# Performance work log

Hardware: AMD Instinct MI355X
Metric: run time of the kernel (lower is better)

## Reference

```python
import jax, jax.numpy as jnp
import numpy as np

# Screen config (matches init_kwargs)
W, H, TL = 1920, 1080, 16
NBW = -(-W // TL)          # 120
NBH = -(-H // TL)          # 68
NB = NBW * NBH             # 8160 tiles
N = 500_000                # number of points
K = 5                      # max tiles per axis a point can overlap (radius < 24, TL=16)
RADIUS_MAX = 24.0


def setup_inputs() -> dict:
    key = jax.random.key(0)
    k1, k2, k3 = jax.random.split(key, 3)
    pos2d = jax.random.uniform(k1, (N, 2), dtype=jnp.float32) * jnp.array([W, H], dtype=jnp.float32)
    radius = jax.random.uniform(k2, (N,), dtype=jnp.float32) * (RADIUS_MAX - 1.0) + 1.0
    depth = jax.random.normal(k3, (N,), dtype=jnp.float32)
    return {"pos2d": pos2d, "radius": radius, "depth": depth}


def reference(pos2d, radius, depth):
    # Tile bounds per point (identical clamping semantics to the torch module).
    xmin = jnp.clip(jnp.floor_divide(pos2d[:, 0] - radius, TL), 0, NBW).astype(jnp.int32)
    ymin = jnp.clip(jnp.floor_divide(pos2d[:, 1] - radius, TL), 0, NBH).astype(jnp.int32)
    xmax = jnp.clip(jnp.floor_divide(pos2d[:, 0] + radius, TL) + 1, 0, NBW).astype(jnp.int32)
    ymax = jnp.clip(jnp.floor_divide(pos2d[:, 1] + radius, TL) + 1, 0, NBH).astype(jnp.int32)

    # Enumerate a fixed KxK candidate tile window per point, mask out-of-range tiles.
    dxy = jnp.arange(K, dtype=jnp.int32)
    xi = xmin[:, None] + dxy            # [N, K]
    yi = ymin[:, None] + dxy            # [N, K]
    vx = xi < xmax[:, None]
    vy = yi < ymax[:, None]
    valid = (vx[:, :, None] & vy[:, None, :]).reshape(-1)              # [E]
    tid = (xi[:, :, None] * NBH + yi[:, None, :]).reshape(-1)          # [E] flat tile id (x-major, as in module)
    tid = jnp.where(valid, tid, NB).astype(jnp.int32)                  # sentinel NB -> sorts to end
    pid = jnp.broadcast_to(jnp.arange(N, dtype=jnp.int32)[:, None, None], (N, K, K)).reshape(-1)
    d_entry = jnp.broadcast_to(depth[:, None, None], (N, K, K)).reshape(-1)

    # Counting-sort equivalent: per-tile histogram + exclusive cumsum offsets.
    counts = jax.ops.segment_sum(valid.astype(jnp.int32), tid, num_segments=NB + 1)[:NB]
    tile_count = jnp.concatenate([jnp.zeros((1,), jnp.int32), jnp.cumsum(counts)[:-1].astype(jnp.int32)])

    # Sort pairs by (tile id, depth descending) -> contiguous per-tile, depth-sorted index lists.
    order = jnp.lexsort((-d_entry, tid))
    tid_s = tid[order]
    pid_s = pid[order]
    live = tid_s < NB
    tile_indices = jnp.where(live, pid_s, -1)                          # padded with -1 at the tail
    sorted_depth = jnp.where(live, depth[pid_s], 0.0)                  # depths in per-tile sorted order
    return tile_count, tile_indices, sorted_depth
```

## Files before the change

### kernel.cpp

```cpp
#include <hip/hip_runtime.h>
#include <stdint.h>
#include <math.h>

typedef unsigned int u32;
typedef unsigned long long u64;

#define NBW 120
#define NBH 68
#define NTILES (NBW * NBH)
#define NPTS 500000
#define EE 12500000
#define SORT_CAP 2048
#define NBKT 1024
#define HB 256
#define HT 512
#define DX 121
#define DY 69
#define DCELLS 8352
#define PCW 4080
#define DSLICE (HB * DCELLS)
#define PCSLICE (HB * PCW)

__device__ __forceinline__ int clampi(int v, int lo, int hi) {
    return v < lo ? lo : (v > hi ? hi : v);
}

__device__ __forceinline__ void tile_window(float x, float y, float r,
                                            int& x0, int& x1, int& y0, int& y1) {
    x0 = clampi((int)floorf((x - r) * 0.0625f), 0, NBW);
    x1 = clampi((int)floorf((x + r) * 0.0625f) + 1, 0, NBW);
    y0 = clampi((int)floorf((y - r) * 0.0625f), 0, NBH);
    y1 = clampi((int)floorf((y + r) * 0.0625f) + 1, 0, NBH);
}

__device__ __forceinline__ u32 depth_key(float d) {
    u32 fu = __float_as_uint(d);
    u32 asc = (fu & 0x80000000u) ? ~fu : (fu | 0x80000000u);
    return ~asc;
}
__device__ __forceinline__ float depth_unkey(u32 dk) {
    u32 asc = ~dk;
    u32 fu = (asc & 0x80000000u) ? (asc & 0x7FFFFFFFu) : ~asc;
    return __uint_as_float(fu);
}

__device__ __forceinline__ int tile_of_block(int b) {
    return (b & 7) * (NTILES / 8) + (b >> 3);
}

__device__ __forceinline__ u32 bucket_of(u32 dk, const u32* __restrict__ Ts) {
    u32 k = dk >> 24;
    u32 t0 = Ts[k], t1 = Ts[k + 1];
    u32 b = t0 + (((t1 - t0) * ((dk >> 8) & 0xFFFFu)) >> 16);
    return b >= NBKT ? (NBKT - 1) : b;
}

__device__ __forceinline__ void lds_inc16(u32* arr, int cell) {
    atomicAdd(&arr[cell >> 1], (cell & 1) ? 0x10000u : 1u);
}

__global__ __launch_bounds__(HT) void hist_kernel(const float2* __restrict__ pos,
                                                  const float* __restrict__ rad,
                                                  u32* __restrict__ pcslc,
                                                  int* __restrict__ diffslc) {
    __shared__ u32 s_pc[PCW];
    __shared__ u32 s_dp[DCELLS / 2];
    __shared__ u32 s_dm[DCELLS / 2];
    int tid = threadIdx.x;
    for (int w = tid; w < PCW; w += HT) s_pc[w] = 0;
    for (int w = tid; w < DCELLS / 2; w += HT) { s_dp[w] = 0; s_dm[w] = 0; }
    __syncthreads();

    for (int i = blockIdx.x * HT + tid; i < NPTS; i += HB * HT) {
        float2 p = pos[i];
        float r = rad[i];
        int x0, x1, y0, y1;
        tile_window(p.x, p.y, r, x0, x1, y0, y1);
        int cx = (int)(p.x * 0.0625f);
        int cy = (int)(p.y * 0.0625f);
        lds_inc16(s_pc, cx * NBH + cy);
        lds_inc16(s_dp, x0 * DY + y0);
        lds_inc16(s_dp, x1 * DY + y1);
        lds_inc16(s_dm, x0 * DY + y1);
        lds_inc16(s_dm, x1 * DY + y0);
    }
    __syncthreads();

    for (int w = tid; w < PCW; w += HT) pcslc[blockIdx.x * PCW + w] = s_pc[w];
    for (int c = tid; c < DCELLS; c += HT) {
        u32 pw = s_dp[c >> 1], mw = s_dm[c >> 1];
        int sh = (c & 1) * 16;
        diffslc[blockIdx.x * DCELLS + c] =
            (int)((pw >> sh) & 0xFFFFu) - (int)((mw >> sh) & 0xFFFFu);
    }
}

__global__ void reduce_kernel(const u32* __restrict__ pcslc, const int* __restrict__ diffslc,
                              u32* __restrict__ counts, u32* __restrict__ ctab0,
                              int* __restrict__ sdg) {
    int idx = blockIdx.x * 256 + threadIdx.x;
    if (idx < NTILES) {
        int sh = (idx & 1) * 16;
        int w = idx >> 1;
        u32 run = 0;
        for (int b = 0; b < HB; ++b) {
            ctab0[b * NTILES + idx] = run;
            run += (pcslc[b * PCW + w] >> sh) & 0xFFFFu;
        }
        counts[idx] = run;
    } else if (idx < NTILES + DCELLS) {
        int c = idx - NTILES;
        int acc = 0;
        for (int b = 0; b < HB; ++b) acc += diffslc[b * DCELLS + c];
        sdg[c] = acc;
    }
}

__global__ __launch_bounds__(1024) void scan3_kernel(const u32* __restrict__ counts,
                                                     u32* __restrict__ po,
                                                     const int* __restrict__ sdg,
                                                     u32* __restrict__ eo,
                                                     float* __restrict__ out_count,
                                                     u32* __restrict__ Tg) {
    __shared__ u32 sA[1024], sB[1024];
    __shared__ int sd[DCELLS];
    __shared__ u32 traw[257];
    int t = threadIdx.x;
    int base = t * 8;

    if (blockIdx.x == 0) {
        u32 local[8]; u32 sum = 0;
#pragma unroll
        for (int j = 0; j < 8; ++j) {
            u32 c = (base + j < NTILES) ? counts[base + j] : 0u;
            local[j] = c; sum += c;
        }
        sA[t] = sum;
        __syncthreads();
        u32 *cur = sA, *nxt = sB;
        for (int off = 1; off < 1024; off <<= 1) {
            u32 v = cur[t];
            if (t >= off) v += cur[t - off];
            nxt[t] = v;
            __syncthreads();
            u32* tmp = cur; cur = nxt; nxt = tmp;
        }
        u32 run = cur[t] - sum;
#pragma unroll
        for (int j = 0; j < 8; ++j) {
            int idx = base + j;
            if (idx < NTILES) { po[idx] = run; run += local[j]; }
        }
        if (t == 1023) po[NTILES] = cur[1023];
    } else if (blockIdx.x == 1) {
        for (int c = t; c < DCELLS; c += 1024) sd[c] = sdg[c];
        __syncthreads();
        if (t < DX) { int run = 0; for (int y = 0; y < DY; ++y) { run += sd[t * DY + y]; sd[t * DY + y] = run; } }
        __syncthreads();
        if (t < DY) { int run = 0; for (int x = 0; x < DX; ++x) { run += sd[x * DY + t]; sd[x * DY + t] = run; } }
        __syncthreads();

        u32 local[8]; u32 sum = 0;
#pragma unroll
        for (int j = 0; j < 8; ++j) {
            int idx = base + j;
            u32 c = 0;
            if (idx < NTILES) {
                int x = idx / NBH, y = idx % NBH;
                c = (u32)sd[x * DY + y];
            }
            local[j] = c; sum += c;
        }
        sA[t] = sum;
        __syncthreads();
        u32 *cur = sA, *nxt = sB;
        for (int off = 1; off < 1024; off <<= 1) {
            u32 v = cur[t];
            if (t >= off) v += cur[t - off];
            nxt[t] = v;
            __syncthreads();
            u32* tmp = cur; cur = nxt; nxt = tmp;
        }
        u32 run = cur[t] - sum;
#pragma unroll
        for (int j = 0; j < 8; ++j) {
            int idx = base + j;
            if (idx < NTILES) {
                eo[idx] = run;
                out_count[idx] = (float)run;
                run += local[j];
            }
        }
        if (t == 1023) eo[NTILES] = cur[1023];
    } else {
        if (t < 257) {
            u32 dkb = (u32)t << 24;
            float d = depth_unkey(dkb);
            float u;
            if (d != d) u = (t < 128) ? 0.f : 1.f;
            else {
                float dc = fminf(fmaxf(d, -12.f), 12.f);
                u = 0.5f * erfcf(dc * 0.70710678f);
            }
            traw[t] = (u32)(u * (float)NBKT + 0.5f);
        }
        __syncthreads();
        if (t == 0) {
            u32 run = 0;
            for (int k = 0; k < 257; ++k) {
                u32 v = traw[k];
                if (v > NBKT) v = NBKT;
                if (v > run) run = v;
                Tg[k] = run;
            }
        }
    }
}

__global__ __launch_bounds__(HT) void point_scatter_kernel(const float2* __restrict__ pos,
                                                           const float* __restrict__ rad,
                                                           const float* __restrict__ depth,
                                                           const u32* __restrict__ ctab0,
                                                           const u32* __restrict__ po,
                                                           ulonglong2* __restrict__ pe16) {
    __shared__ u32 cur[NTILES];
    int tid = threadIdx.x;
    for (int w = tid; w < NTILES; w += HT)
        cur[w] = ctab0[blockIdx.x * NTILES + w] + po[w];
    __syncthreads();
    for (int i = blockIdx.x * HT + tid; i < NPTS; i += HB * HT) {
        float2 p = pos[i];
        float r = rad[i];
        int x0, x1, y0, y1;
        tile_window(p.x, p.y, r, x0, x1, y0, y1);
        int cx = (int)(p.x * 0.0625f);
        int cy = (int)(p.y * 0.0625f);
        u32 dk = depth_key(depth[i]);
        u32 w = (u32)x0 | ((u32)y0 << 7) | ((u32)x1 << 14) | ((u32)y1 << 21);
        u32 slot = atomicAdd(&cur[cx * NBH + cy], 1u);
        pe16[slot] = make_ulonglong2(((u64)dk << 19) | (u64)(u32)i, (u64)w);
    }
}

__global__ __launch_bounds__(256) void tile_build_kernel(const u32* __restrict__ po,
                                                         const ulonglong2* __restrict__ pe16,
                                                         const u32* __restrict__ eo,
                                                         const u32* __restrict__ Tg,
                                                         float* __restrict__ out_idx,
                                                         float* __restrict__ out_depth) {
    __shared__ u64 keys[SORT_CAP];
    __shared__ u32 boff[NBKT + 1];
    __shared__ u32 bcur[NBKT];
    __shared__ u32 Ts[257];
    __shared__ u32 wsum[4];
    __shared__ u32 lcnt;

    int tid = threadIdx.x;
    int lane = tid & 63;
    int wv = tid >> 6;

    {
        u32 total = eo[NTILES];
        u32 tailn = EE - total;
        u32 per = (tailn + NTILES - 1) / NTILES;
        u64 s = (u64)total + (u64)blockIdx.x * per;
        u64 e = s + per; if (e > (u64)EE) e = EE;
        for (u64 i = s + tid; i < e; i += 256) {
            out_idx[i] = -1.f;
            out_depth[i] = 0.f;
        }
    }

    int t = tile_of_block(blockIdx.x);
    u32 base = eo[t];
    int cnt = (int)(eo[t + 1] - base);
    if (cnt <= 0) return;

    int tx = t / NBH;
    int ty = t % NBH;
    bool big = cnt > SORT_CAP;

    for (int b = tid; b < NBKT; b += 256) boff[b] = 0;
    for (int k = tid; k < 257; k += 256) Ts[k] = Tg[k];
    if (tid == 0) lcnt = 0;
    __syncthreads();

    int cx0 = tx - 2 < 0 ? 0 : tx - 2;
    int cx1 = tx + 2 > NBW - 1 ? NBW - 1 : tx + 2;
    int cy0 = ty - 2 < 0 ? 0 : ty - 2;
    int cy1 = ty + 2 > NBH - 1 ? NBH - 1 : ty + 2;

    if (!big) {
        for (int cx = cx0; cx <= cx1; ++cx) {
            u32 s = po[cx * NBH + cy0];
            u32 e = po[cx * NBH + cy1 + 1];
            for (u32 i = s + tid; i < e; i += 256) {
                ulonglong2 en = pe16[i];
                u32 w = (u32)en.y;
                int x0 = (int)(w & 127u), y0 = (int)((w >> 7) & 127u);
                int x1 = (int)((w >> 14) & 127u), y1 = (int)((w >> 21) & 127u);
                if (tx >= x0 && tx < x1 && ty >= y0 && ty < y1) {
                    u32 dk = (u32)(en.x >> 19);
                    atomicAdd(&boff[bucket_of(dk, Ts)], 1u);
                }
            }
        }
        __syncthreads();

        {
            int b0 = tid * 4;
            u32 h0 = boff[b0], h1 = boff[b0 + 1], h2 = boff[b0 + 2], h3 = boff[b0 + 3];
            u32 tsum = h0 + h1 + h2 + h3;
            u32 v = tsum;
            for (int off = 1; off < 64; off <<= 1) {
                u32 n = __shfl_up(v, off, 64);
                if (lane >= off) v += n;
            }
            if (lane == 63) wsum[wv] = v;
            __syncthreads();
            u32 wpre = 0;
            for (int w = 0; w < wv; ++w) wpre += wsum[w];
            u32 run = wpre + v - tsum;
            boff[b0] = run;     bcur[b0] = run;     run += h0;
            boff[b0 + 1] = run; bcur[b0 + 1] = run; run += h1;
            boff[b0 + 2] = run; bcur[b0 + 2] = run; run += h2;
            boff[b0 + 3] = run; bcur[b0 + 3] = run; run += h3;
            if (tid == 255) boff[NBKT] = run;
        }
        __syncthreads();

        for (int cx = cx0; cx <= cx1; ++cx) {
            u32 s = po[cx * NBH + cy0];
            u32 e = po[cx * NBH + cy1 + 1];
            for (u32 i = s + tid; i < e; i += 256) {
                ulonglong2 en = pe16[i];
                u32 w = (u32)en.y;
                int x0 = (int)(w & 127u), y0 = (int)((w >> 7) & 127u);
                int x1 = (int)((w >> 14) & 127u), y1 = (int)((w >> 21) & 127u);
                if (tx >= x0 && tx < x1 && ty >= y0 && ty < y1) {
                    u32 dk = (u32)(en.x >> 19);
                    u32 slot = atomicAdd(&bcur[bucket_of(dk, Ts)], 1u);
                    keys[slot] = en.x;
                }
            }
        }
        __syncthreads();

        for (int b = tid; b < NBKT; b += 256) {
            int s = (int)boff[b], e = (int)boff[b + 1];
            for (int i = s + 1; i < e; ++i) {
                u64 k = keys[i];
                int j = i - 1;
                while (j >= s && keys[j] > k) { keys[j + 1] = keys[j]; --j; }
                keys[j + 1] = k;
            }
        }
        __syncthreads();

        for (int i = tid; i < cnt; i += 256) {
            u64 k = keys[i];
            u32 pid = (u32)(k & 0x7FFFFu);
            u32 dk  = (u32)(k >> 19);
            out_idx[base + i]   = (float)pid;
            out_depth[base + i] = depth_unkey(dk);
        }
    } else {
        for (int cx = cx0; cx <= cx1; ++cx) {
            u32 s = po[cx * NBH + cy0];
            u32 e = po[cx * NBH + cy1 + 1];
            for (u32 i = s + tid; i < e; i += 256) {
                ulonglong2 en = pe16[i];
                u32 w = (u32)en.y;
                int x0 = (int)(w & 127u), y0 = (int)((w >> 7) & 127u);
                int x1 = (int)((w >> 14) & 127u), y1 = (int)((w >> 21) & 127u);
                if (tx >= x0 && tx < x1 && ty >= y0 && ty < y1) {
                    u32 pid = (u32)(en.x & 0x7FFFFu);
                    u32 dk  = (u32)(en.x >> 19);
                    u32 slot = atomicAdd(&lcnt, 1u);
                    out_idx[base + slot] = (float)pid;
                    out_depth[base + slot] = depth_unkey(dk);
                }
            }
        }
        __syncthreads();
        for (int round = 0; round < cnt; ++round) {
            for (int i = (round & 1) + 2 * tid; i + 1 < cnt; i += 512) {
                float fi0 = out_idx[base + i], fi1 = out_idx[base + i + 1];
                float fd0 = out_depth[base + i], fd1 = out_depth[base + i + 1];
                u64 k0 = ((u64)depth_key(fd0) << 19) | (u64)(u32)fi0;
                u64 k1 = ((u64)depth_key(fd1) << 19) | (u64)(u32)fi1;
                if (k0 > k1) {
                    out_idx[base + i] = fi1; out_idx[base + i + 1] = fi0;
                    out_depth[base + i] = fd1; out_depth[base + i + 1] = fd0;
                }
            }
            __syncthreads();
        }
    }
}

extern "C" void kernel_launch(void* const* d_in, const int* in_sizes, int n_in,
                              void* d_out, int out_size, void* d_ws, size_t ws_size,
                              hipStream_t stream) {
    (void)in_sizes; (void)n_in; (void)out_size; (void)ws_size;

    const float2* pos  = (const float2*)d_in[0];
    const float* rad   = (const float*)d_in[1];
    const float* depth = (const float*)d_in[2];

    float* out        = (float*)d_out;
    float* out_count  = out;
    float* out_idx    = out + NTILES;
    float* out_depth  = out + NTILES + EE;

    ulonglong2* pe16 = (ulonglong2*)d_ws;
    u32* counts = (u32*)(pe16 + NPTS);
    u32* po     = counts + NTILES;
    u32* eo     = po + NTILES + 1;
    int* sdg    = (int*)(eo + NTILES + 1);
    u32* Tg     = (u32*)(sdg + DCELLS);

    u32* ctab0   = (u32*)out_idx + (EE - HB * NTILES);
    u32* pcslc   = (u32*)(out_depth + EE) - (PCSLICE + DSLICE);
    int* diffslc = (int*)(pcslc + PCSLICE);

    hist_kernel<<<HB, HT, 0, stream>>>(pos, rad, pcslc, diffslc);
    reduce_kernel<<<(NTILES + DCELLS + 255) / 256, 256, 0, stream>>>(pcslc, diffslc,
                                                                     counts, ctab0, sdg);
    scan3_kernel<<<3, 1024, 0, stream>>>(counts, po, sdg, eo, out_count, Tg);
    point_scatter_kernel<<<HB, HT, 0, stream>>>(pos, rad, depth, ctab0, po, pe16);
    tile_build_kernel<<<NTILES, 256, 0, stream>>>(po, pe16, eo, Tg,
                                                  out_idx, out_depth);
}
```

Baseline: 221.5 us.

## Fuse histogram, reduce, scan and scatter into one cooperative kernel

Merges the four preprocessing kernels (per-block histogram, slice reduce, scans, point scatter) into a single cooperative kernel separated by grid syncs. Each thread keeps its per-point tile cell, depth key and window in registers, so the scatter phase no longer reloads pos, radius and depth. Per-block prefix tables are shrunk to 16-bit and the difference slices are packed two per word, which halves that scratch traffic. The costs are the cooperative launch, three grid-wide barriers, and idle blocks during the scan phase, which now runs on 512 threads.

```diff
diff --git a/kernel.cpp b/kernel.cpp
--- a/kernel.cpp
+++ b/kernel.cpp
@@ -1,7 +1,11 @@
 #include <hip/hip_runtime.h>
+#include <hip/hip_cooperative_groups.h>
 #include <stdint.h>
 #include <math.h>
 
+namespace cg = cooperative_groups;
+
+typedef unsigned short u16;
 typedef unsigned int u32;
 typedef unsigned long long u64;
 
@@ -14,12 +18,13 @@
 #define NBKT 1024
 #define HB 256
 #define HT 512
+#define PPT 4
 #define DX 121
 #define DY 69
 #define DCELLS 8352
+#define DCW (DCELLS / 2)
 #define PCW 4080
-#define DSLICE (HB * DCELLS)
-#define PCSLICE (HB * PCW)
+#define SMEMW (PCW + DCELLS)
 
 __device__ __forceinline__ int clampi(int v, int lo, int hi) {
     return v < lo ? lo : (v > hi ? hi : v);
@@ -59,110 +64,124 @@
     atomicAdd(&arr[cell >> 1], (cell & 1) ? 0x10000u : 1u);
 }
 
-__global__ __launch_bounds__(HT) void hist_kernel(const float2* __restrict__ pos,
-                                                  const float* __restrict__ rad,
-                                                  u32* __restrict__ pcslc,
-                                                  int* __restrict__ diffslc) {
-    __shared__ u32 s_pc[PCW];
-    __shared__ u32 s_dp[DCELLS / 2];
-    __shared__ u32 s_dm[DCELLS / 2];
+__global__ __launch_bounds__(HT) void prep_kernel(
+    const float2* __restrict__ pos, const float* __restrict__ rad,
+    const float* __restrict__ depth,
+    u32* __restrict__ pcslc, u32* __restrict__ diffslc,
+    u16* __restrict__ ctab0, u32* __restrict__ counts,
+    u32* __restrict__ po, int* __restrict__ sdg,
+    u32* __restrict__ eo, float* __restrict__ out_count,
+    u32* __restrict__ Tg, ulonglong2* __restrict__ pe16)
+{
+    cg::grid_group grid = cg::this_grid();
+    __shared__ u32 smem[SMEMW];
     int tid = threadIdx.x;
-    for (int w = tid; w < PCW; w += HT) s_pc[w] = 0;
-    for (int w = tid; w < DCELLS / 2; w += HT) { s_dp[w] = 0; s_dm[w] = 0; }
-    __syncthreads();
-
-    for (int i = blockIdx.x * HT + tid; i < NPTS; i += HB * HT) {
-        float2 p = pos[i];
-        float r = rad[i];
-        int x0, x1, y0, y1;
-        tile_window(p.x, p.y, r, x0, x1, y0, y1);
-        int cx = (int)(p.x * 0.0625f);
-        int cy = (int)(p.y * 0.0625f);
-        lds_inc16(s_pc, cx * NBH + cy);
-        lds_inc16(s_dp, x0 * DY + y0);
-        lds_inc16(s_dp, x1 * DY + y1);
-        lds_inc16(s_dm, x0 * DY + y1);
-        lds_inc16(s_dm, x1 * DY + y0);
-    }
-    __syncthreads();
-
-    for (int w = tid; w < PCW; w += HT) pcslc[blockIdx.x * PCW + w] = s_pc[w];
-    for (int c = tid; c < DCELLS; c += HT) {
-        u32 pw = s_dp[c >> 1], mw = s_dm[c >> 1];
-        int sh = (c & 1) * 16;
-        diffslc[blockIdx.x * DCELLS + c] =
-            (int)((pw >> sh) & 0xFFFFu) - (int)((mw >> sh) & 0xFFFFu);
-    }
-}
-
-__global__ void reduce_kernel(const u32* __restrict__ pcslc, const int* __restrict__ diffslc,
-                              u32* __restrict__ counts, u32* __restrict__ ctab0,
-                              int* __restrict__ sdg) {
-    int idx = blockIdx.x * 256 + threadIdx.x;
-    if (idx < NTILES) {
-        int sh = (idx & 1) * 16;
-        int w = idx >> 1;
-        u32 run = 0;
-        for (int b = 0; b < HB; ++b) {
-            ctab0[b * NTILES + idx] = run;
-            run += (pcslc[b * PCW + w] >> sh) & 0xFFFFu;
-        }
-        counts[idx] = run;
-    } else if (idx < NTILES + DCELLS) {
-        int c = idx - NTILES;
-        int acc = 0;
-        for (int b = 0; b < HB; ++b) acc += diffslc[b * DCELLS + c];
-        sdg[c] = acc;
-    }
-}
-
-__global__ __launch_bounds__(1024) void scan3_kernel(const u32* __restrict__ counts,
-                                                     u32* __restrict__ po,
-                                                     const int* __restrict__ sdg,
-                                                     u32* __restrict__ eo,
-                                                     float* __restrict__ out_count,
-                                                     u32* __restrict__ Tg) {
-    __shared__ u32 sA[1024], sB[1024];
-    __shared__ int sd[DCELLS];
-    __shared__ u32 traw[257];
-    int t = threadIdx.x;
-    int base = t * 8;
-
-    if (blockIdx.x == 0) {
-        u32 local[8]; u32 sum = 0;
-#pragma unroll
-        for (int j = 0; j < 8; ++j) {
+    int b = blockIdx.x;
+
+    u32 rw[PPT], rct[PPT], rdk[PPT];
+    {
+        u32* s_pc = smem;
+        u32* s_dp = smem + PCW;
+        u32* s_dm = smem + PCW + DCW;
+        for (int w = tid; w < SMEMW; w += HT) smem[w] = 0;
+        __syncthreads();
+
+#pragma unroll
+        for (int k = 0; k < PPT; ++k) {
+            int i = b * HT + tid + k * (HB * HT);
+            rct[k] = 0xFFFFFFFFu;
+            if (i < NPTS) {
+                float2 p = pos[i];
+                float r = rad[i];
+                int x0, x1, y0, y1;
+                tile_window(p.x, p.y, r, x0, x1, y0, y1);
+                int cx = (int)(p.x * 0.0625f);
+                int cy = (int)(p.y * 0.0625f);
+                rct[k] = (u32)(cx * NBH + cy);
+                rdk[k] = depth_key(depth[i]);
+                rw[k]  = (u32)x0 | ((u32)y0 << 7) | ((u32)x1 << 14) | ((u32)y1 << 21);
+                lds_inc16(s_pc, (int)rct[k]);
+                lds_inc16(s_dp, x0 * DY + y0);
+                lds_inc16(s_dp, x1 * DY + y1);
+                lds_inc16(s_dm, x0 * DY + y1);
+                lds_inc16(s_dm, x1 * DY + y0);
+            }
+        }
+        __syncthreads();
+
+        for (int w = tid; w < PCW; w += HT) pcslc[b * PCW + w] = s_pc[w];
+        for (int wi = tid; wi < DCW; wi += HT) {
+            u32 pw = s_dp[wi], mw = s_dm[wi];
+            int d0 = (int)(pw & 0xFFFFu) - (int)(mw & 0xFFFFu);
+            int d1 = (int)(pw >> 16)     - (int)(mw >> 16);
+            diffslc[b * DCW + wi] = ((u32)d0 & 0xFFFFu) | ((u32)d1 << 16);
+        }
+    }
+    grid.sync();
+
+    {
+        int g = b * HT + tid;
+        if (g < NTILES) {
+            int w = g >> 1, sh = (g & 1) * 16;
+            u32 run = 0;
+            for (int s = 0; s < HB; ++s) {
+                ctab0[s * NTILES + g] = (u16)run;
+                run += (pcslc[s * PCW + w] >> sh) & 0xFFFFu;
+            }
+            counts[g] = run;
+        } else if (g < NTILES + DCELLS) {
+            int c = g - NTILES;
+            int wi = c >> 1, sh = (c & 1) * 16;
+            int acc = 0;
+            for (int s = 0; s < HB; ++s)
+                acc += (int)(short)((diffslc[s * DCW + wi] >> sh) & 0xFFFFu);
+            sdg[c] = acc;
+        }
+    }
+    grid.sync();
+
+    if (b == 0) {
+        u32* sA = smem;
+        u32* sB = smem + 512;
+        int base = tid * 16;
+        u32 local[16]; u32 sum = 0;
+#pragma unroll
+        for (int j = 0; j < 16; ++j) {
             u32 c = (base + j < NTILES) ? counts[base + j] : 0u;
             local[j] = c; sum += c;
         }
-        sA[t] = sum;
-        __syncthreads();
-        u32 *cur = sA, *nxt = sB;
-        for (int off = 1; off < 1024; off <<= 1) {
-            u32 v = cur[t];
-            if (t >= off) v += cur[t - off];
-            nxt[t] = v;
+        sA[tid] = sum;
+        __syncthreads();
+        u32 *curp = sA, *nxt = sB;
+        for (int off = 1; off < 512; off <<= 1) {
+            u32 v = curp[tid];
+            if (tid >= off) v += curp[tid - off];
+            nxt[tid] = v;
             __syncthreads();
-            u32* tmp = cur; cur = nxt; nxt = tmp;
-        }
-        u32 run = cur[t] - sum;
-#pragma unroll
-        for (int j = 0; j < 8; ++j) {
+            u32* tmp = curp; curp = nxt; nxt = tmp;
+        }
+        u32 run = curp[tid] - sum;
+#pragma unroll
+        for (int j = 0; j < 16; ++j) {
             int idx = base + j;
             if (idx < NTILES) { po[idx] = run; run += local[j]; }
         }
-        if (t == 1023) po[NTILES] = cur[1023];
-    } else if (blockIdx.x == 1) {
-        for (int c = t; c < DCELLS; c += 1024) sd[c] = sdg[c];
-        __syncthreads();
-        if (t < DX) { int run = 0; for (int y = 0; y < DY; ++y) { run += sd[t * DY + y]; sd[t * DY + y] = run; } }
-        __syncthreads();
-        if (t < DY) { int run = 0; for (int x = 0; x < DX; ++x) { run += sd[x * DY + t]; sd[x * DY + t] = run; } }
-        __syncthreads();
-
-        u32 local[8]; u32 sum = 0;
-#pragma unroll
-        for (int j = 0; j < 8; ++j) {
+        if (tid == 511) po[NTILES] = curp[511];
+    } else if (b == 1) {
+        int* sd = (int*)smem;
+        u32* sA = smem + DCELLS;
+        u32* sB = sA + 512;
+        for (int c = tid; c < DCELLS; c += HT) sd[c] = sdg[c];
+        __syncthreads();
+        if (tid < DX) { int run = 0; for (int y = 0; y < DY; ++y) { run += sd[tid * DY + y]; sd[tid * DY + y] = run; } }
+        __syncthreads();
+        if (tid < DY) { int run = 0; for (int x = 0; x < DX; ++x) { run += sd[x * DY + tid]; sd[x * DY + tid] = run; } }
+        __syncthreads();
+
+        int base = tid * 16;
+        u32 local[16]; u32 sum = 0;
+#pragma unroll
+        for (int j = 0; j < 16; ++j) {
             int idx = base + j;
             u32 c = 0;
             if (idx < NTILES) {
@@ -171,19 +190,19 @@
             }
             local[j] = c; sum += c;
         }
-        sA[t] = sum;
-        __syncthreads();
-        u32 *cur = sA, *nxt = sB;
-        for (int off = 1; off < 1024; off <<= 1) {
-            u32 v = cur[t];
-            if (t >= off) v += cur[t - off];
-            nxt[t] = v;
+        sA[tid] = sum;
+        __syncthreads();
+        u32 *curp = sA, *nxt = sB;
+        for (int off = 1; off < 512; off <<= 1) {
+            u32 v = curp[tid];
+            if (tid >= off) v += curp[tid - off];
+            nxt[tid] = v;
             __syncthreads();
-            u32* tmp = cur; cur = nxt; nxt = tmp;
-        }
-        u32 run = cur[t] - sum;
-#pragma unroll
-        for (int j = 0; j < 8; ++j) {
+            u32* tmp = curp; curp = nxt; nxt = tmp;
+        }
+        u32 run = curp[tid] - sum;
+#pragma unroll
+        for (int j = 0; j < 16; ++j) {
             int idx = base + j;
             if (idx < NTILES) {
                 eo[idx] = run;
@@ -191,21 +210,22 @@
                 run += local[j];
             }
         }
-        if (t == 1023) eo[NTILES] = cur[1023];
-    } else {
-        if (t < 257) {
-            u32 dkb = (u32)t << 24;
+        if (tid == 511) eo[NTILES] = curp[511];
+    } else if (b == 2) {
+        u32* traw = smem;
+        if (tid < 257) {
+            u32 dkb = (u32)tid << 24;
             float d = depth_unkey(dkb);
             float u;
-            if (d != d) u = (t < 128) ? 0.f : 1.f;
+            if (d != d) u = (tid < 128) ? 0.f : 1.f;
             else {
                 float dc = fminf(fmaxf(d, -12.f), 12.f);
                 u = 0.5f * erfcf(dc * 0.70710678f);
             }
-            traw[t] = (u32)(u * (float)NBKT + 0.5f);
-        }
-        __syncthreads();
-        if (t == 0) {
+            traw[tid] = (u32)(u * (float)NBKT + 0.5f);
+        }
+        __syncthreads();
+        if (tid == 0) {
             u32 run = 0;
             for (int k = 0; k < 257; ++k) {
                 u32 v = traw[k];
@@ -215,30 +235,22 @@
             }
         }
     }
-}
-
-__global__ __launch_bounds__(HT) void point_scatter_kernel(const float2* __restrict__ pos,
-                                                           const float* __restrict__ rad,
-                                                           const float* __restrict__ depth,
-                                                           const u32* __restrict__ ctab0,
-                                                           const u32* __restrict__ po,
-                                                           ulonglong2* __restrict__ pe16) {
-    __shared__ u32 cur[NTILES];
-    int tid = threadIdx.x;
-    for (int w = tid; w < NTILES; w += HT)
-        cur[w] = ctab0[blockIdx.x * NTILES + w] + po[w];
-    __syncthreads();
-    for (int i = blockIdx.x * HT + tid; i < NPTS; i += HB * HT) {
-        float2 p = pos[i];
-        float r = rad[i];
-        int x0, x1, y0, y1;
-        tile_window(p.x, p.y, r, x0, x1, y0, y1);
-        int cx = (int)(p.x * 0.0625f);
-        int cy = (int)(p.y * 0.0625f);
-        u32 dk = depth_key(depth[i]);
-        u32 w = (u32)x0 | ((u32)y0 << 7) | ((u32)x1 << 14) | ((u32)y1 << 21);
-        u32 slot = atomicAdd(&cur[cx * NBH + cy], 1u);
-        pe16[slot] = make_ulonglong2(((u64)dk << 19) | (u64)(u32)i, (u64)w);
+    grid.sync();
+
+    {
+        u32* cur = smem;
+        for (int w = tid; w < NTILES; w += HT)
+            cur[w] = po[w] + (u32)ctab0[b * NTILES + w];
+        __syncthreads();
+#pragma unroll
+        for (int k = 0; k < PPT; ++k) {
+            if (rct[k] != 0xFFFFFFFFu) {
+                int i = b * HT + tid + k * (HB * HT);
+                u32 slot = atomicAdd(&cur[rct[k]], 1u);
+                pe16[slot] = make_ulonglong2(((u64)rdk[k] << 19) | (u64)(u32)i,
+                                             (u64)rw[k]);
+            }
+        }
     }
 }
 
@@ -420,15 +432,18 @@
     int* sdg    = (int*)(eo + NTILES + 1);
     u32* Tg     = (u32*)(sdg + DCELLS);
 
-    u32* ctab0   = (u32*)out_idx + (EE - HB * NTILES);
-    u32* pcslc   = (u32*)(out_depth + EE) - (PCSLICE + DSLICE);
-    int* diffslc = (int*)(pcslc + PCSLICE);
-
-    hist_kernel<<<HB, HT, 0, stream>>>(pos, rad, pcslc, diffslc);
-    reduce_kernel<<<(NTILES + DCELLS + 255) / 256, 256, 0, stream>>>(pcslc, diffslc,
-                                                                     counts, ctab0, sdg);
-    scan3_kernel<<<3, 1024, 0, stream>>>(counts, po, sdg, eo, out_count, Tg);
-    point_scatter_kernel<<<HB, HT, 0, stream>>>(pos, rad, depth, ctab0, po, pe16);
+    u16* ctab0   = (u16*)((u32*)out_idx + EE) - (size_t)HB * NTILES;
+    u32* pcslc   = (u32*)(out_depth + EE) - ((size_t)HB * PCW + (size_t)HB * DCW);
+    u32* diffslc = pcslc + (size_t)HB * PCW;
+
+    void* kargs[] = {
+        (void*)&pos, (void*)&rad, (void*)&depth,
+        (void*)&pcslc, (void*)&diffslc, (void*)&ctab0, (void*)&counts,
+        (void*)&po, (void*)&sdg, (void*)&eo, (void*)&out_count,
+        (void*)&Tg, (void*)&pe16
+    };
+    hipLaunchCooperativeKernel(reinterpret_cast<void*>(prep_kernel),
+                               dim3(HB), dim3(HT), kargs, 0, stream);
     tile_build_kernel<<<NTILES, 256, 0, stream>>>(po, pe16, eo, Tg,
                                                   out_idx, out_depth);
 }
```

New measurement: 307.7 us. 38.9% more time.

## Pack point entries into 64-bit words and halve intermediate histogram tables

Applied to the files above, without the earlier changes.

Per-point scatter entries shrink from 16 bytes to 8 by encoding the tile window relative to the home cell (dx0, dx1, y0, height) alongside the depth key and point id. The per-block prefix table becomes 16-bit, and the signed diff slices are packed two per word. This cuts global traffic in the tile-build gather, which rereads neighbour entries many times, and in the reduce and scatter setup. The packing assumes each window spans at most 4 tiles per axis relative to the centre cell and that per-tile per-block counts fit in 16 bits.

```diff
diff --git a/kernel.cpp b/kernel.cpp
--- a/kernel.cpp
+++ b/kernel.cpp
@@ -2,6 +2,7 @@
 #include <stdint.h>
 #include <math.h>
 
+typedef unsigned short u16;
 typedef unsigned int u32;
 typedef unsigned long long u64;
 
@@ -17,9 +18,8 @@
 #define DX 121
 #define DY 69
 #define DCELLS 8352
+#define DCW (DCELLS / 2)
 #define PCW 4080
-#define DSLICE (HB * DCELLS)
-#define PCSLICE (HB * PCW)
 
 __device__ __forceinline__ int clampi(int v, int lo, int hi) {
     return v < lo ? lo : (v > hi ? hi : v);
@@ -59,16 +59,17 @@
     atomicAdd(&arr[cell >> 1], (cell & 1) ? 0x10000u : 1u);
 }
 
+
 __global__ __launch_bounds__(HT) void hist_kernel(const float2* __restrict__ pos,
                                                   const float* __restrict__ rad,
                                                   u32* __restrict__ pcslc,
-                                                  int* __restrict__ diffslc) {
+                                                  u32* __restrict__ diffslc) {
     __shared__ u32 s_pc[PCW];
-    __shared__ u32 s_dp[DCELLS / 2];
-    __shared__ u32 s_dm[DCELLS / 2];
+    __shared__ u32 s_dp[DCW];
+    __shared__ u32 s_dm[DCW];
     int tid = threadIdx.x;
     for (int w = tid; w < PCW; w += HT) s_pc[w] = 0;
-    for (int w = tid; w < DCELLS / 2; w += HT) { s_dp[w] = 0; s_dm[w] = 0; }
+    for (int w = tid; w < DCW; w += HT) { s_dp[w] = 0; s_dm[w] = 0; }
     __syncthreads();
 
     for (int i = blockIdx.x * HT + tid; i < NPTS; i += HB * HT) {
@@ -87,16 +88,16 @@
     __syncthreads();
 
     for (int w = tid; w < PCW; w += HT) pcslc[blockIdx.x * PCW + w] = s_pc[w];
-    for (int c = tid; c < DCELLS; c += HT) {
-        u32 pw = s_dp[c >> 1], mw = s_dm[c >> 1];
-        int sh = (c & 1) * 16;
-        diffslc[blockIdx.x * DCELLS + c] =
-            (int)((pw >> sh) & 0xFFFFu) - (int)((mw >> sh) & 0xFFFFu);
-    }
-}
-
-__global__ void reduce_kernel(const u32* __restrict__ pcslc, const int* __restrict__ diffslc,
-                              u32* __restrict__ counts, u32* __restrict__ ctab0,
+    for (int wi = tid; wi < DCW; wi += HT) {
+        u32 pw = s_dp[wi], mw = s_dm[wi];
+        int d0 = (int)(pw & 0xFFFFu) - (int)(mw & 0xFFFFu);
+        int d1 = (int)(pw >> 16)     - (int)(mw >> 16);
+        diffslc[blockIdx.x * DCW + wi] = ((u32)d0 & 0xFFFFu) | ((u32)d1 << 16);
+    }
+}
+
+__global__ void reduce_kernel(const u32* __restrict__ pcslc, const u32* __restrict__ diffslc,
+                              u32* __restrict__ counts, u16* __restrict__ ctab0,
                               int* __restrict__ sdg) {
     int idx = blockIdx.x * 256 + threadIdx.x;
     if (idx < NTILES) {
@@ -104,14 +105,16 @@
         int w = idx >> 1;
         u32 run = 0;
         for (int b = 0; b < HB; ++b) {
-            ctab0[b * NTILES + idx] = run;
+            ctab0[b * NTILES + idx] = (u16)run;
             run += (pcslc[b * PCW + w] >> sh) & 0xFFFFu;
         }
         counts[idx] = run;
     } else if (idx < NTILES + DCELLS) {
         int c = idx - NTILES;
+        int wi = c >> 1, sh = (c & 1) * 16;
         int acc = 0;
-        for (int b = 0; b < HB; ++b) acc += diffslc[b * DCELLS + c];
+        for (int b = 0; b < HB; ++b)
+            acc += (int)(short)((diffslc[b * DCW + wi] >> sh) & 0xFFFFu);
         sdg[c] = acc;
     }
 }
@@ -220,13 +223,13 @@
 __global__ __launch_bounds__(HT) void point_scatter_kernel(const float2* __restrict__ pos,
                                                            const float* __restrict__ rad,
                                                            const float* __restrict__ depth,
-                                                           const u32* __restrict__ ctab0,
+                                                           const u16* __restrict__ ctab0,
                                                            const u32* __restrict__ po,
-                                                           ulonglong2* __restrict__ pe16) {
+                                                           u64* __restrict__ pe) {
     __shared__ u32 cur[NTILES];
     int tid = threadIdx.x;
     for (int w = tid; w < NTILES; w += HT)
-        cur[w] = ctab0[blockIdx.x * NTILES + w] + po[w];
+        cur[w] = po[w] + (u32)ctab0[blockIdx.x * NTILES + w];
     __syncthreads();
     for (int i = blockIdx.x * HT + tid; i < NPTS; i += HB * HT) {
         float2 p = pos[i];
@@ -236,14 +239,15 @@
         int cx = (int)(p.x * 0.0625f);
         int cy = (int)(p.y * 0.0625f);
         u32 dk = depth_key(depth[i]);
-        u32 w = (u32)x0 | ((u32)y0 << 7) | ((u32)x1 << 14) | ((u32)y1 << 21);
+        u32 meta = ((u32)(cx - x0) << 11) | ((u32)(x1 - cx - 1) << 9)
+                 | ((u32)y0 << 2) | (u32)(y1 - y0 - 1);
         u32 slot = atomicAdd(&cur[cx * NBH + cy], 1u);
-        pe16[slot] = make_ulonglong2(((u64)dk << 19) | (u64)(u32)i, (u64)w);
+        pe[slot] = ((u64)dk << 32) | ((u64)(u32)i << 13) | (u64)meta;
     }
 }
 
 __global__ __launch_bounds__(256) void tile_build_kernel(const u32* __restrict__ po,
-                                                         const ulonglong2* __restrict__ pe16,
+                                                         const u64* __restrict__ pe,
                                                          const u32* __restrict__ eo,
                                                          const u32* __restrict__ Tg,
                                                          float* __restrict__ out_idx,
@@ -292,15 +296,18 @@
 
     if (!big) {
         for (int cx = cx0; cx <= cx1; ++cx) {
+            int dcx = cx - tx;
             u32 s = po[cx * NBH + cy0];
             u32 e = po[cx * NBH + cy1 + 1];
             for (u32 i = s + tid; i < e; i += 256) {
-                ulonglong2 en = pe16[i];
-                u32 w = (u32)en.y;
-                int x0 = (int)(w & 127u), y0 = (int)((w >> 7) & 127u);
-                int x1 = (int)((w >> 14) & 127u), y1 = (int)((w >> 21) & 127u);
-                if (tx >= x0 && tx < x1 && ty >= y0 && ty < y1) {
-                    u32 dk = (u32)(en.x >> 19);
+                u64 v = pe[i];
+                u32 meta = (u32)v & 0x1FFFu;
+                int h = (int)(meta & 3u);
+                int y0 = (int)((meta >> 2) & 127u);
+                int dx1m1 = (int)((meta >> 9) & 3u);
+                int dx0 = (int)((meta >> 11) & 3u);
+                if (dx0 >= dcx && dx1m1 >= -dcx && ty >= y0 && ty <= y0 + h) {
+                    u32 dk = (u32)(v >> 32);
                     atomicAdd(&boff[bucket_of(dk, Ts)], 1u);
                 }
             }
@@ -330,17 +337,20 @@
         __syncthreads();
 
         for (int cx = cx0; cx <= cx1; ++cx) {
+            int dcx = cx - tx;
             u32 s = po[cx * NBH + cy0];
             u32 e = po[cx * NBH + cy1 + 1];
             for (u32 i = s + tid; i < e; i += 256) {
-                ulonglong2 en = pe16[i];
-                u32 w = (u32)en.y;
-                int x0 = (int)(w & 127u), y0 = (int)((w >> 7) & 127u);
-                int x1 = (int)((w >> 14) & 127u), y1 = (int)((w >> 21) & 127u);
-                if (tx >= x0 && tx < x1 && ty >= y0 && ty < y1) {
-                    u32 dk = (u32)(en.x >> 19);
+                u64 v = pe[i];
+                u32 meta = (u32)v & 0x1FFFu;
+                int h = (int)(meta & 3u);
+                int y0 = (int)((meta >> 2) & 127u);
+                int dx1m1 = (int)((meta >> 9) & 3u);
+                int dx0 = (int)((meta >> 11) & 3u);
+                if (dx0 >= dcx && dx1m1 >= -dcx && ty >= y0 && ty <= y0 + h) {
+                    u32 dk = (u32)(v >> 32);
                     u32 slot = atomicAdd(&bcur[bucket_of(dk, Ts)], 1u);
-                    keys[slot] = en.x;
+                    keys[slot] = v;
                 }
             }
         }
@@ -359,23 +369,26 @@
 
         for (int i = tid; i < cnt; i += 256) {
             u64 k = keys[i];
-            u32 pid = (u32)(k & 0x7FFFFu);
-            u32 dk  = (u32)(k >> 19);
+            u32 pid = (u32)(k >> 13) & 0x7FFFFu;
+            u32 dk  = (u32)(k >> 32);
             out_idx[base + i]   = (float)pid;
             out_depth[base + i] = depth_unkey(dk);
         }
     } else {
         for (int cx = cx0; cx <= cx1; ++cx) {
+            int dcx = cx - tx;
             u32 s = po[cx * NBH + cy0];
             u32 e = po[cx * NBH + cy1 + 1];
             for (u32 i = s + tid; i < e; i += 256) {
-                ulonglong2 en = pe16[i];
-                u32 w = (u32)en.y;
-                int x0 = (int)(w & 127u), y0 = (int)((w >> 7) & 127u);
-                int x1 = (int)((w >> 14) & 127u), y1 = (int)((w >> 21) & 127u);
-                if (tx >= x0 && tx < x1 && ty >= y0 && ty < y1) {
-                    u32 pid = (u32)(en.x & 0x7FFFFu);
-                    u32 dk  = (u32)(en.x >> 19);
+                u64 v = pe[i];
+                u32 meta = (u32)v & 0x1FFFu;
+                int h = (int)(meta & 3u);
+                int y0 = (int)((meta >> 2) & 127u);
+                int dx1m1 = (int)((meta >> 9) & 3u);
+                int dx0 = (int)((meta >> 11) & 3u);
+                if (dx0 >= dcx && dx1m1 >= -dcx && ty >= y0 && ty <= y0 + h) {
+                    u32 pid = (u32)(v >> 13) & 0x7FFFFu;
+                    u32 dk  = (u32)(v >> 32);
                     u32 slot = atomicAdd(&lcnt, 1u);
                     out_idx[base + slot] = (float)pid;
                     out_depth[base + slot] = depth_unkey(dk);
@@ -413,22 +426,22 @@
     float* out_idx    = out + NTILES;
     float* out_depth  = out + NTILES + EE;
 
-    ulonglong2* pe16 = (ulonglong2*)d_ws;
-    u32* counts = (u32*)(pe16 + NPTS);
+    u64* pe     = (u64*)d_ws;
+    u32* counts = (u32*)(pe + NPTS);
     u32* po     = counts + NTILES;
     u32* eo     = po + NTILES + 1;
     int* sdg    = (int*)(eo + NTILES + 1);
     u32* Tg     = (u32*)(sdg + DCELLS);
 
-    u32* ctab0   = (u32*)out_idx + (EE - HB * NTILES);
-    u32* pcslc   = (u32*)(out_depth + EE) - (PCSLICE + DSLICE);
-    int* diffslc = (int*)(pcslc + PCSLICE);
+    u16* ctab0   = (u16*)((u32*)out_idx + EE) - (size_t)HB * NTILES;
+    u32* pcslc   = (u32*)(out_depth + EE) - ((size_t)HB * PCW + (size_t)HB * DCW);
+    u32* diffslc = pcslc + (size_t)HB * PCW;
 
     hist_kernel<<<HB, HT, 0, stream>>>(pos, rad, pcslc, diffslc);
     reduce_kernel<<<(NTILES + DCELLS + 255) / 256, 256, 0, stream>>>(pcslc, diffslc,
                                                                      counts, ctab0, sdg);
     scan3_kernel<<<3, 1024, 0, stream>>>(counts, po, sdg, eo, out_count, Tg);
-    point_scatter_kernel<<<HB, HT, 0, stream>>>(pos, rad, depth, ctab0, po, pe16);
-    tile_build_kernel<<<NTILES, 256, 0, stream>>>(po, pe16, eo, Tg,
+    point_scatter_kernel<<<HB, HT, 0, stream>>>(pos, rad, depth, ctab0, po, pe);
+    tile_build_kernel<<<NTILES, 256, 0, stream>>>(po, pe, eo, Tg,
                                                   out_idx, out_depth);
 }
```

Measured after the change: 224.5 us. No clear change (+1.4%).
